# Performance work log

Measured on AMD Instinct MI355X. Metric: run time of the kernel, lower is better.

The kernel has to match this reference:

```python
import jax, jax.numpy as jnp
import numpy as np

N, P, E, H = 64, 1024, 512, 8
R = E // H  # head dim


def _xavier(key, shape, dtype=jnp.float32):
    fan_in, fan_out = shape[-1], shape[-2] if len(shape) > 1 else shape[-1]
    lim = jnp.sqrt(6.0 / (fan_in + fan_out)).astype(dtype)
    return jax.random.uniform(key, shape, dtype, -lim, lim)


def setup_inputs() -> dict:
    key = jax.random.key(0)
    k1, k2, k3, k4 = jax.random.split(key, 4)
    x = jax.random.normal(k1, (N, P, E), dtype=jnp.float32)
    alpha = _xavier(k2, (H, P))          # translation-invariant attention weights
    V = _xavier(k3, (H, R, E))           # per-head value projection
    W = _xavier(k4, (E, E))              # Dense kernel
    b = jnp.zeros((E,), dtype=jnp.float32)  # Dense bias
    return {"x": x, "alpha": alpha, "V": V, "W": W, "b": b}


def _log_cosh(x):
    # log(cosh(x)) = |x| + log1p(exp(-2|x|)) - log(2), numerically stable
    ax = jnp.abs(x)
    return ax + jnp.log1p(jnp.exp(-2.0 * ax)) - jnp.log(2.0).astype(x.dtype)


def reference(x, alpha, V, W, b):
    n, p, e = x.shape
    # circulant matrix: alpha_mat[h, i, j] = alpha[h, (j - i) mod P]
    # (equivalent to stacking jnp.roll(alpha, shift=i) over i)
    idx = (jnp.arange(p)[None, :] - jnp.arange(p)[:, None]) % p  # (P, P)
    alpha_mat = alpha[:, idx]                                    # (H, P, P)
    ws = jnp.einsum('hrd,npd->nhpr', V, x)                       # (N, H, P, R)
    y = jnp.einsum('hpj,nhjr->nphr', alpha_mat, ws)              # (N, P, H, R)
    y = y.reshape(n, p, -1)                                      # (N, P, E)
    y = y @ W + b
    return _log_cosh(y)
```

## Files before the change

kernel.cpp:

```cpp
#include <hip/hip_runtime.h>
#include <math.h>

typedef float f32x4 __attribute__((ext_vector_type(4)));
typedef __bf16 bf16x8 __attribute__((ext_vector_type(8)));
typedef unsigned short u16x8 __attribute__((ext_vector_type(8)));
typedef unsigned short u16x4 __attribute__((ext_vector_type(4)));

#define LN2F_ 0.69314718055994530942f

__device__ inline unsigned short f2bf(float f) {
    unsigned u = __builtin_bit_cast(unsigned, f);
    u += 0x7fffu + ((u >> 16) & 1u);
    return (unsigned short)(u >> 16);
}

__device__ inline void stage_st(unsigned short* Ls, int row, int c, u16x8 v) {
    *(u16x8*)(Ls + (row >> 4) * 512 + (((c) << 4) + ((row & 15) ^ ((c) << 1))) * 8) = v;
}
__device__ inline bf16x8 frag_ld(const unsigned short* Ls, int s, int ml, int q) {
    return __builtin_bit_cast(bf16x8,
        *(const u16x8*)(Ls + s * 512 + (((q) << 4) + (ml ^ ((q) << 1))) * 8));
}

__global__ __launch_bounds__(256) void k_cvt(const float* __restrict__ in,
                                             unsigned short* __restrict__ out, int n4) {
    int i = blockIdx.x * 256 + threadIdx.x;
    if (i >= n4) return;
    float4 v = ((const float4*)in)[i];
    u16x4 o = { f2bf(v.x), f2bf(v.y), f2bf(v.z), f2bf(v.w) };
    *(u16x4*)(out + (size_t)i * 4) = o;
}

__global__ __launch_bounds__(256) void k_build_am(const float* __restrict__ alpha,
                                                  unsigned short* __restrict__ am) {
    int t = blockIdx.x * 256 + threadIdx.x;
    int j8 = (t & 127) << 3;
    int p  = (t >> 7) & 1023;
    int h  = t >> 17;
    const float* ar = alpha + (h << 10);
    u16x8 o;
#pragma unroll
    for (int q = 0; q < 8; ++q) o[q] = f2bf(ar[(j8 + q - p) & 1023]);
    *(u16x8*)(am + ((size_t)t << 3)) = o;
}

__global__ __launch_bounds__(256) void k_build_wt(const float* __restrict__ W,
                                                  unsigned short* __restrict__ WT) {
    int t = blockIdx.x * 256 + threadIdx.x;
    int e1 = t >> 9, e = t & 511;
    WT[t] = f2bf(W[e * 512 + e1]);
}

__global__ __launch_bounds__(256) void k_gemm1(const float* __restrict__ X,
                                               const unsigned short* __restrict__ B,
                                               unsigned short* __restrict__ wsT) {
    __shared__ __align__(16) unsigned short As[128 * 32];
    __shared__ __align__(16) unsigned short Bs[128 * 32];
    const int tid = threadIdx.x;
    const int flat = blockIdx.x;
    const int xcd = flat & 7, slot = flat >> 3;
    const int m0 = (xcd * 64 + (slot >> 2)) * 128;
    const int e0 = (slot & 3) * 128;
    const int w = tid >> 6, lane = tid & 63, ml = lane & 15, quad = lane >> 4;
    const int wr = w >> 1, wc = w & 1;
    const int srow = tid >> 1, shalf = tid & 1;
    f32x4 acc[4][4] = {};
    for (int k0 = 0; k0 < 512; k0 += 32) {
        const float* ap = X + (size_t)(m0 + srow) * 512 + k0 + shalf * 16;
        float4 a0 = ((const float4*)ap)[0];
        float4 a1 = ((const float4*)ap)[1];
        float4 a2 = ((const float4*)ap)[2];
        float4 a3 = ((const float4*)ap)[3];
        const unsigned short* bp = B + (size_t)(e0 + srow) * 512 + k0 + shalf * 16;
        u16x8 rb0 = *(const u16x8*)bp;
        u16x8 rb1 = *(const u16x8*)(bp + 8);
        __syncthreads();
        u16x8 pa0 = { f2bf(a0.x), f2bf(a0.y), f2bf(a0.z), f2bf(a0.w),
                      f2bf(a1.x), f2bf(a1.y), f2bf(a1.z), f2bf(a1.w) };
        u16x8 pa1 = { f2bf(a2.x), f2bf(a2.y), f2bf(a2.z), f2bf(a2.w),
                      f2bf(a3.x), f2bf(a3.y), f2bf(a3.z), f2bf(a3.w) };
        stage_st(As, srow, shalf * 2 + 0, pa0);
        stage_st(As, srow, shalf * 2 + 1, pa1);
        stage_st(Bs, srow, shalf * 2 + 0, rb0);
        stage_st(Bs, srow, shalf * 2 + 1, rb1);
        __syncthreads();
        bf16x8 af[4], bfr[4];
#pragma unroll
        for (int i = 0; i < 4; ++i) {
            af[i]  = frag_ld(As, wr * 4 + i, ml, quad);
            bfr[i] = frag_ld(Bs, wc * 4 + i, ml, quad);
        }
#pragma unroll
        for (int i = 0; i < 4; ++i)
#pragma unroll
            for (int j = 0; j < 4; ++j)
                acc[i][j] = __builtin_amdgcn_mfma_f32_16x16x32_bf16(af[i], bfr[j], acc[i][j], 0, 0, 0);
    }
    const int n = m0 >> 10;
    const int pblk = m0 & 1023;
#pragma unroll
    for (int i = 0; i < 4; ++i) {
        int p = pblk + wr * 64 + i * 16 + quad * 4;
#pragma unroll
        for (int j = 0; j < 4; ++j) {
            int e = e0 + wc * 64 + j * 16 + ml;
            u16x4 o = { f2bf(acc[i][j][0]), f2bf(acc[i][j][1]),
                        f2bf(acc[i][j][2]), f2bf(acc[i][j][3]) };
            *(u16x4*)(wsT + ((size_t)n * 512 + e) * 1024 + p) = o;
        }
    }
}

__global__ __launch_bounds__(512) void k_gemm2(const unsigned short* __restrict__ wsT,
                                               const unsigned short* __restrict__ am,
                                               unsigned short* __restrict__ y) {
    __shared__ __align__(16) unsigned short As[256 * 32];
    __shared__ __align__(16) unsigned short Bs[128 * 32];
    const int tid = threadIdx.x;
    const int flat = blockIdx.x;
    const int xcd = flat & 7, slot = flat >> 3;
    const int panel = xcd * 16 + (slot >> 3);
    const int p0 = (slot & 7) * 128;
    const int h  = panel & 7;
    const int n0 = (panel >> 3) * 4;
    const int w = tid >> 6, lane = tid & 63, ml = lane & 15, quad = lane >> 4;
    const int wn = w >> 1, wp = w & 1;
    const int arow = tid >> 1, ahalf = tid & 1;
    const int brow = tid >> 2, bc = tid & 3;
    const unsigned short* Ap = wsT + (size_t)(n0 + (arow >> 6)) * 524288
                                   + (size_t)(h * 64 + (arow & 63)) * 1024 + ahalf * 16;
    const unsigned short* Bp = am + ((size_t)h * 1024 + p0 + brow) * 1024 + bc * 8;
    f32x4 acc[4][4] = {};
    for (int j0 = 0; j0 < 1024; j0 += 32) {
        u16x8 ra0 = *(const u16x8*)(Ap + j0);
        u16x8 ra1 = *(const u16x8*)(Ap + j0 + 8);
        u16x8 rb  = *(const u16x8*)(Bp + j0);
        __syncthreads();
        stage_st(As, arow, ahalf * 2 + 0, ra0);
        stage_st(As, arow, ahalf * 2 + 1, ra1);
        stage_st(Bs, brow, bc, rb);
        __syncthreads();
        bf16x8 af[4], bfr[4];
#pragma unroll
        for (int mt = 0; mt < 4; ++mt)
            af[mt] = frag_ld(As, wn * 4 + mt, ml, quad);
#pragma unroll
        for (int nt = 0; nt < 4; ++nt)
            bfr[nt] = frag_ld(Bs, wp * 4 + nt, ml, quad);
#pragma unroll
        for (int mt = 0; mt < 4; ++mt)
#pragma unroll
            for (int nt = 0; nt < 4; ++nt)
                acc[mt][nt] = __builtin_amdgcn_mfma_f32_16x16x32_bf16(af[mt], bfr[nt], acc[mt][nt], 0, 0, 0);
    }
    const int n = n0 + wn;
#pragma unroll
    for (int mt = 0; mt < 4; ++mt) {
        int r0 = mt * 16 + quad * 4;
#pragma unroll
        for (int nt = 0; nt < 4; ++nt) {
            int p = p0 + wp * 64 + nt * 16 + ml;
            u16x4 o = { f2bf(acc[mt][nt][0]), f2bf(acc[mt][nt][1]),
                        f2bf(acc[mt][nt][2]), f2bf(acc[mt][nt][3]) };
            *(u16x4*)(y + ((size_t)n * 1024 + p) * 512 + h * 64 + r0) = o;
        }
    }
}

__global__ __launch_bounds__(256) void k_gemm3(const unsigned short* __restrict__ A,
                                               const unsigned short* __restrict__ B,
                                               const float* __restrict__ bias,
                                               float* __restrict__ out) {
    __shared__ __align__(16) unsigned short As[128 * 32];
    __shared__ __align__(16) unsigned short Bs[128 * 32];
    const int tid = threadIdx.x;
    const int flat = blockIdx.x;
    const int xcd = flat & 7, slot = flat >> 3;
    const int m0 = (xcd * 64 + (slot >> 2)) * 128;
    const int e0 = (slot & 3) * 128;
    const int w = tid >> 6, lane = tid & 63, ml = lane & 15, quad = lane >> 4;
    const int wr = w >> 1, wc = w & 1;
    const int srow = tid >> 1, shalf = tid & 1;
    f32x4 acc[4][4] = {};
    for (int k0 = 0; k0 < 512; k0 += 32) {
        const unsigned short* ap = A + (size_t)(m0 + srow) * 512 + k0 + shalf * 16;
        u16x8 ra0 = *(const u16x8*)ap;
        u16x8 ra1 = *(const u16x8*)(ap + 8);
        const unsigned short* bp = B + (size_t)(e0 + srow) * 512 + k0 + shalf * 16;
        u16x8 rb0 = *(const u16x8*)bp;
        u16x8 rb1 = *(const u16x8*)(bp + 8);
        __syncthreads();
        stage_st(As, srow, shalf * 2 + 0, ra0);
        stage_st(As, srow, shalf * 2 + 1, ra1);
        stage_st(Bs, srow, shalf * 2 + 0, rb0);
        stage_st(Bs, srow, shalf * 2 + 1, rb1);
        __syncthreads();
        bf16x8 af[4], bfr[4];
#pragma unroll
        for (int i = 0; i < 4; ++i) {
            af[i]  = frag_ld(As, wr * 4 + i, ml, quad);
            bfr[i] = frag_ld(Bs, wc * 4 + i, ml, quad);
        }
#pragma unroll
        for (int i = 0; i < 4; ++i)
#pragma unroll
            for (int j = 0; j < 4; ++j)
                acc[i][j] = __builtin_amdgcn_mfma_f32_16x16x32_bf16(af[i], bfr[j], acc[i][j], 0, 0, 0);
    }
#pragma unroll
    for (int j = 0; j < 4; ++j) {
        int e = e0 + wc * 64 + j * 16 + ml;
        float bv = bias[e];
#pragma unroll
        for (int i = 0; i < 4; ++i) {
            int mg = m0 + wr * 64 + i * 16 + quad * 4;
#pragma unroll
            for (int r = 0; r < 4; ++r) {
                float v  = acc[i][j][r] + bv;
                float ax = fabsf(v);
                float t  = __expf(-2.0f * ax);
                out[(size_t)(mg + r) * 512 + e] = ax + __logf(1.0f + t) - LN2F_;
            }
        }
    }
}

extern "C" void kernel_launch(void* const* d_in, const int* in_sizes, int n_in,
                              void* d_out, int out_size, void* d_ws, size_t ws_size,
                              hipStream_t stream) {
    const float* x     = (const float*)d_in[0];
    const float* alpha = (const float*)d_in[1];
    const float* V     = (const float*)d_in[2];
    const float* W     = (const float*)d_in[3];
    const float* b     = (const float*)d_in[4];

    unsigned short* am  = (unsigned short*)d_out;
    unsigned short* Vb  = am + 8388608;
    unsigned short* wsT = (unsigned short*)d_ws;
    unsigned short* y   = wsT + 33554432;
    unsigned short* WT  = wsT;
    float* out = (float*)d_out;

    k_cvt<<<256, 256, 0, stream>>>(V, Vb, 65536);
    k_build_am<<<4096, 256, 0, stream>>>(alpha, am);

    k_gemm1<<<dim3(2048), 256, 0, stream>>>(x, Vb, wsT);
    k_gemm2<<<dim3(1024), 512, 0, stream>>>(wsT, am, y);
    k_build_wt<<<1024, 256, 0, stream>>>(W, WT);
    k_gemm3<<<dim3(2048), 256, 0, stream>>>(y, WT, b, out);
}
```

Measured before the change: 453.6 us.

## Stage GEMM tiles via direct global-to-LDS loads and pre-convert x to bf16

All three GEMM kernels now fill their LDS tiles with global_load_lds 16-byte transfers instead of loading into registers and storing to LDS. The swizzle is moved into the per-lane source row selection. Because direct loads cannot convert types, x is first turned into bf16 by a separate conversion pass that writes a buffer carved out of the output region. This removes register staging and conversion ALU work from the inner loops, but adds a full extra read and write pass over x.

```diff
diff --git a/kernel.cpp b/kernel.cpp
--- a/kernel.cpp
+++ b/kernel.cpp
@@ -14,12 +14,15 @@
     return (unsigned short)(u >> 16);
 }
 
-__device__ inline void stage_st(unsigned short* Ls, int row, int c, u16x8 v) {
-    *(u16x8*)(Ls + (row >> 4) * 512 + (((c) << 4) + ((row & 15) ^ ((c) << 1))) * 8) = v;
-}
 __device__ inline bf16x8 frag_ld(const unsigned short* Ls, int s, int ml, int q) {
     return __builtin_bit_cast(bf16x8,
         *(const u16x8*)(Ls + s * 512 + (((q) << 4) + (ml ^ ((q) << 1))) * 8));
+}
+
+__device__ inline void gll16(const unsigned short* g, unsigned short* l) {
+    __builtin_amdgcn_global_load_lds(
+        (const __attribute__((address_space(1))) unsigned int*)g,
+        (__attribute__((address_space(3))) unsigned int*)l, 16, 0, 0);
 }
 
 __global__ __launch_bounds__(256) void k_cvt(const float* __restrict__ in,
@@ -51,7 +54,7 @@
     WT[t] = f2bf(W[e * 512 + e1]);
 }
 
-__global__ __launch_bounds__(256) void k_gemm1(const float* __restrict__ X,
+__global__ __launch_bounds__(256) void k_gemm1(const unsigned short* __restrict__ A,
                                                const unsigned short* __restrict__ B,
                                                unsigned short* __restrict__ wsT) {
     __shared__ __align__(16) unsigned short As[128 * 32];
@@ -63,26 +66,23 @@
     const int e0 = (slot & 3) * 128;
     const int w = tid >> 6, lane = tid & 63, ml = lane & 15, quad = lane >> 4;
     const int wr = w >> 1, wc = w & 1;
-    const int srow = tid >> 1, shalf = tid & 1;
+    const int srl = (lane & 15) ^ ((lane >> 4) << 1);
+    const int scl = lane >> 4;
+    const unsigned short* pA0 = A + (size_t)(m0 + w * 32 + srl) * 512 + scl * 8;
+    const unsigned short* pA1 = pA0 + 16 * 512;
+    const unsigned short* pB0 = B + (size_t)(e0 + w * 32 + srl) * 512 + scl * 8;
+    const unsigned short* pB1 = pB0 + 16 * 512;
+    unsigned short* lA0 = As + w * 1024;
+    unsigned short* lA1 = lA0 + 512;
+    unsigned short* lB0 = Bs + w * 1024;
+    unsigned short* lB1 = lB0 + 512;
     f32x4 acc[4][4] = {};
     for (int k0 = 0; k0 < 512; k0 += 32) {
-        const float* ap = X + (size_t)(m0 + srow) * 512 + k0 + shalf * 16;
-        float4 a0 = ((const float4*)ap)[0];
-        float4 a1 = ((const float4*)ap)[1];
-        float4 a2 = ((const float4*)ap)[2];
-        float4 a3 = ((const float4*)ap)[3];
-        const unsigned short* bp = B + (size_t)(e0 + srow) * 512 + k0 + shalf * 16;
-        u16x8 rb0 = *(const u16x8*)bp;
-        u16x8 rb1 = *(const u16x8*)(bp + 8);
-        __syncthreads();
-        u16x8 pa0 = { f2bf(a0.x), f2bf(a0.y), f2bf(a0.z), f2bf(a0.w),
-                      f2bf(a1.x), f2bf(a1.y), f2bf(a1.z), f2bf(a1.w) };
-        u16x8 pa1 = { f2bf(a2.x), f2bf(a2.y), f2bf(a2.z), f2bf(a2.w),
-                      f2bf(a3.x), f2bf(a3.y), f2bf(a3.z), f2bf(a3.w) };
-        stage_st(As, srow, shalf * 2 + 0, pa0);
-        stage_st(As, srow, shalf * 2 + 1, pa1);
-        stage_st(Bs, srow, shalf * 2 + 0, rb0);
-        stage_st(Bs, srow, shalf * 2 + 1, rb1);
+        __syncthreads();
+        gll16(pA0 + k0, lA0);
+        gll16(pA1 + k0, lA1);
+        gll16(pB0 + k0, lB0);
+        gll16(pB1 + k0, lB1);
         __syncthreads();
         bf16x8 af[4], bfr[4];
 #pragma unroll
@@ -125,20 +125,22 @@
     const int n0 = (panel >> 3) * 4;
     const int w = tid >> 6, lane = tid & 63, ml = lane & 15, quad = lane >> 4;
     const int wn = w >> 1, wp = w & 1;
-    const int arow = tid >> 1, ahalf = tid & 1;
-    const int brow = tid >> 2, bc = tid & 3;
-    const unsigned short* Ap = wsT + (size_t)(n0 + (arow >> 6)) * 524288
-                                   + (size_t)(h * 64 + (arow & 63)) * 1024 + ahalf * 16;
-    const unsigned short* Bp = am + ((size_t)h * 1024 + p0 + brow) * 1024 + bc * 8;
+    const int srl = (lane & 15) ^ ((lane >> 4) << 1);
+    const int scl = lane >> 4;
+    const unsigned short* pA0 = wsT + (size_t)(n0 + (w >> 1)) * 524288
+        + (size_t)(h * 64 + ((2 * w) & 3) * 16 + srl) * 1024 + scl * 8;
+    const unsigned short* pA1 = wsT + (size_t)(n0 + (w >> 1)) * 524288
+        + (size_t)(h * 64 + ((2 * w + 1) & 3) * 16 + srl) * 1024 + scl * 8;
+    const unsigned short* pB = am + ((size_t)h * 1024 + p0 + w * 16 + srl) * 1024 + scl * 8;
+    unsigned short* lA0 = As + (2 * w) * 512;
+    unsigned short* lA1 = lA0 + 512;
+    unsigned short* lB  = Bs + w * 512;
     f32x4 acc[4][4] = {};
     for (int j0 = 0; j0 < 1024; j0 += 32) {
-        u16x8 ra0 = *(const u16x8*)(Ap + j0);
-        u16x8 ra1 = *(const u16x8*)(Ap + j0 + 8);
-        u16x8 rb  = *(const u16x8*)(Bp + j0);
-        __syncthreads();
-        stage_st(As, arow, ahalf * 2 + 0, ra0);
-        stage_st(As, arow, ahalf * 2 + 1, ra1);
-        stage_st(Bs, brow, bc, rb);
+        __syncthreads();
+        gll16(pA0 + j0, lA0);
+        gll16(pA1 + j0, lA1);
+        gll16(pB + j0, lB);
         __syncthreads();
         bf16x8 af[4], bfr[4];
 #pragma unroll
@@ -180,20 +182,23 @@
     const int e0 = (slot & 3) * 128;
     const int w = tid >> 6, lane = tid & 63, ml = lane & 15, quad = lane >> 4;
     const int wr = w >> 1, wc = w & 1;
-    const int srow = tid >> 1, shalf = tid & 1;
+    const int srl = (lane & 15) ^ ((lane >> 4) << 1);
+    const int scl = lane >> 4;
+    const unsigned short* pA0 = A + (size_t)(m0 + w * 32 + srl) * 512 + scl * 8;
+    const unsigned short* pA1 = pA0 + 16 * 512;
+    const unsigned short* pB0 = B + (size_t)(e0 + w * 32 + srl) * 512 + scl * 8;
+    const unsigned short* pB1 = pB0 + 16 * 512;
+    unsigned short* lA0 = As + w * 1024;
+    unsigned short* lA1 = lA0 + 512;
+    unsigned short* lB0 = Bs + w * 1024;
+    unsigned short* lB1 = lB0 + 512;
     f32x4 acc[4][4] = {};
     for (int k0 = 0; k0 < 512; k0 += 32) {
-        const unsigned short* ap = A + (size_t)(m0 + srow) * 512 + k0 + shalf * 16;
-        u16x8 ra0 = *(const u16x8*)ap;
-        u16x8 ra1 = *(const u16x8*)(ap + 8);
-        const unsigned short* bp = B + (size_t)(e0 + srow) * 512 + k0 + shalf * 16;
-        u16x8 rb0 = *(const u16x8*)bp;
-        u16x8 rb1 = *(const u16x8*)(bp + 8);
-        __syncthreads();
-        stage_st(As, srow, shalf * 2 + 0, ra0);
-        stage_st(As, srow, shalf * 2 + 1, ra1);
-        stage_st(Bs, srow, shalf * 2 + 0, rb0);
-        stage_st(Bs, srow, shalf * 2 + 1, rb1);
+        __syncthreads();
+        gll16(pA0 + k0, lA0);
+        gll16(pA1 + k0, lA1);
+        gll16(pB0 + k0, lB0);
+        gll16(pB1 + k0, lB1);
         __syncthreads();
         bf16x8 af[4], bfr[4];
 #pragma unroll
@@ -236,15 +241,17 @@
 
     unsigned short* am  = (unsigned short*)d_out;
     unsigned short* Vb  = am + 8388608;
+    unsigned short* Xb  = Vb + 262144;
     unsigned short* wsT = (unsigned short*)d_ws;
     unsigned short* y   = wsT + 33554432;
     unsigned short* WT  = wsT;
     float* out = (float*)d_out;
 
     k_cvt<<<256, 256, 0, stream>>>(V, Vb, 65536);
+    k_cvt<<<32768, 256, 0, stream>>>(x, Xb, 8388608);
     k_build_am<<<4096, 256, 0, stream>>>(alpha, am);
 
-    k_gemm1<<<dim3(2048), 256, 0, stream>>>(x, Vb, wsT);
+    k_gemm1<<<dim3(2048), 256, 0, stream>>>(Xb, Vb, wsT);
     k_gemm2<<<dim3(1024), 512, 0, stream>>>(wsT, am, y);
     k_build_wt<<<1024, 256, 0, stream>>>(W, WT);
     k_gemm3<<<dim3(2048), 256, 0, stream>>>(y, WT, b, out);
```

After: 497.6 us. +9.7%, slower.
